# Kernel tuning notes

Hardware: AMD Instinct MI355X
Metric: run time of the kernel (lower is better)

Reference implementation:

```python
import jax, jax.numpy as jnp
import numpy as np

N, P, E = 100000, 10000, 500000
DN, DP, DK, SKIP, MLP_H = 256, 128, 100, 27, 64
E_MEAN, E_STD = 4.0, 2.0
ETA_MEAN, ETA_STD = 0.0, 1.5
ATT_NORM = 0.1  # 1/sqrt(100)
LN_EPS, RMS_EPS = 1e-5, 1e-6


def setup_inputs() -> dict:
    key = jax.random.key(0)
    ks = jax.random.split(key, 32)
    DIN = DN + SKIP  # 283
    s = 0.05
    inp = {
        'node_hidden': jax.random.normal(ks[0], (N, DN), jnp.float32),
        'energy': jax.random.uniform(ks[1], (N,), jnp.float32, 0.01, 1.0),
        'eta': jax.random.normal(ks[2], (N,), jnp.float32),
        'phi': jax.random.normal(ks[3], (N,), jnp.float32),
        'layer': jax.random.uniform(ks[4], (N,), jnp.float32),
        'eta_l': jax.random.normal(ks[5], (N, 6), jnp.float32),
        'phi_l': jax.random.normal(ks[6], (N, 6), jnp.float32),
        'ene_l': jax.random.normal(ks[7], (N, 6), jnp.float32),
        'track_feats': jax.random.uniform(ks[8], (N, 5), jnp.float32),
        'particle_hidden': jax.random.normal(ks[9], (P, DP), jnp.float32),
        'global_rep': jax.random.normal(ks[10], (P, DN), jnp.float32),
        'edge_src': jax.random.randint(ks[11], (E,), 0, N, jnp.int32),
        'edge_dst': jax.random.randint(ks[12], (E,), 0, P, jnp.int32),
        # learned params
        'W_key': jax.random.normal(ks[13], (DIN, DK), jnp.float32) * s,
        'b_key': jnp.zeros((DK,), jnp.float32),
        'W_val': jax.random.normal(ks[14], (DIN, DP), jnp.float32) * s,
        'b_val': jnp.zeros((DP,), jnp.float32),
        'W_q': jax.random.normal(ks[15], (DP + DN, DK), jnp.float32) * s,
        'b_q': jnp.zeros((DK,), jnp.float32),
        'W_ih': jax.random.normal(ks[16], (DP, 3 * DP), jnp.float32) * s,
        'b_ih': jnp.zeros((3 * DP,), jnp.float32),
        'W_hh': jax.random.normal(ks[17], (DP, 3 * DP), jnp.float32) * s,
        'b_hh': jnp.zeros((3 * DP,), jnp.float32),
        'ln_g': jnp.ones((DP,), jnp.float32),
        'ln_b': jnp.zeros((DP,), jnp.float32),
        'W1': jax.random.normal(ks[18], (DP, MLP_H), jnp.float32) * s,
        'b1': jnp.zeros((MLP_H,), jnp.float32),
        'W2': jax.random.normal(ks[19], (MLP_H, DP), jnp.float32) * s,
        'b2': jnp.zeros((DP,), jnp.float32),
        'rms_w': jnp.ones((DP,), jnp.float32),
        'lin_w': jax.random.normal(ks[20], (1, DP), jnp.float32),
    }
    return inp


def _forward(node_hidden, energy, eta, phi, layer, eta_l, phi_l, ene_l, track_feats,
             particle_hidden, global_rep,
             W_key, b_key, W_val, b_val, W_q, b_q, W_ih, b_ih, W_hh, b_hh,
             ln_g, ln_b, W1, b1, W2, b2, rms_w, lin_w, edge_src, edge_dst):
    # --- build node inputs: hidden rep + 27 skip scalars (same order as torch cat) ---
    skip = jnp.concatenate([
        ((jnp.log(energy) - E_MEAN) / E_STD)[:, None],
        ((eta - ETA_MEAN) / ETA_STD)[:, None],
        phi[:, None], layer[:, None],
        (eta_l - ETA_MEAN) / ETA_STD,  # eta_l1..l6
        phi_l, ene_l,
        track_feats,  # isTrack, nTracks, tracks_pt, nTracks_4, tracks_pt_4
    ], axis=1)  # [N, 27]
    x = jnp.concatenate([node_hidden, skip], axis=1)  # [N, 283]
    keys = x @ W_key + b_key      # [N, 100]
    vals = x @ W_val + b_val      # [N, DP]
    q = jnp.concatenate([particle_hidden, global_rep], axis=1) @ W_q + b_q  # [P, 100]

    # --- per-edge attention (note: node_update consumes RAW relu attention) ---
    att = jax.nn.relu(jnp.sum(keys[edge_src] * q[edge_dst], axis=1) * ATT_NORM)  # [E]
    msg = att[:, None] * vals[edge_src]                                          # [E, DP]
    ws = jax.ops.segment_sum(msg, edge_dst, num_segments=P)                      # [P, DP]

    # --- node update: rmsnorm * sigmoid(eltwise) gating, GRU, LN, MLP residual ---
    rms = ws * jax.lax.rsqrt(jnp.mean(ws * ws, axis=-1, keepdims=True) + RMS_EPS) * rms_w
    gated = rms * jax.nn.sigmoid(ws * lin_w)

    h = particle_hidden
    gi = gated @ W_ih + b_ih
    gh = h @ W_hh + b_hh
    i_r, i_z, i_n = jnp.split(gi, 3, axis=1)
    h_r, h_z, h_n = jnp.split(gh, 3, axis=1)
    r = jax.nn.sigmoid(i_r + h_r)
    z = jax.nn.sigmoid(i_z + h_z)
    n = jnp.tanh(i_n + r * h_n)
    h_new = (1.0 - z) * n + z * h

    mu = jnp.mean(h_new, axis=-1, keepdims=True)
    var = jnp.mean((h_new - mu) ** 2, axis=-1, keepdims=True)
    ln = (h_new - mu) * jax.lax.rsqrt(var + LN_EPS) * ln_g + ln_b
    mlp = jax.nn.relu(ln @ W1 + b1) @ W2 + b2
    return h + mlp  # updated particle 'node hidden rep'


def reference(node_hidden, energy, eta, phi, layer, eta_l, phi_l, ene_l, track_feats,
              particle_hidden, global_rep, edge_src, edge_dst,
              W_key, b_key, W_val, b_val, W_q, b_q, W_ih, b_ih, W_hh, b_hh,
              ln_g, ln_b, W1, b1, W2, b2, rms_w, lin_w):
    return _forward(node_hidden, energy, eta, phi, layer, eta_l, phi_l, ene_l, track_feats,
                    particle_hidden, global_rep,
                    W_key, b_key, W_val, b_val, W_q, b_q, W_ih, b_ih, W_hh, b_hh,
                    ln_g, ln_b, W1, b1, W2, b2, rms_w, lin_w, edge_src, edge_dst)
```

## Files before the change

kernel.cpp:

```cpp
#include <hip/hip_runtime.h>
#include <hip/hip_bf16.h>
#include <math.h>

#define THREADS 256

typedef __bf16 bf16_t;
typedef __bf16 bf16x8 __attribute__((ext_vector_type(8)));
typedef __bf16 bf16x4 __attribute__((ext_vector_type(4)));
typedef float f32x4 __attribute__((ext_vector_type(4)));

__device__ __forceinline__ float sigmoidf_(float x) { return 1.f / (1.f + expf(-x)); }

__device__ __forceinline__ void gload_lds16(const void* g, void* l) {
    __builtin_amdgcn_global_load_lds((const __attribute__((address_space(1))) void*)g,
                                     (__attribute__((address_space(3))) void*)l, 16, 0, 0);
}

__device__ __forceinline__ bf16x8 cvt8(float4 a, float4 b) {
    bf16x8 v;
    v[0] = (bf16_t)a.x; v[1] = (bf16_t)a.y; v[2] = (bf16_t)a.z; v[3] = (bf16_t)a.w;
    v[4] = (bf16_t)b.x; v[5] = (bf16_t)b.y; v[6] = (bf16_t)b.z; v[7] = (bf16_t)b.w;
    return v;
}

__global__ void prep_kernel(const float* __restrict__ W_key, const float* __restrict__ W_val,
                            const float* __restrict__ W_q, const float* __restrict__ b_key,
                            const float* __restrict__ b_val, const float* __restrict__ b_q,
                            bf16_t* __restrict__ WbfT, bf16_t* __restrict__ WqT,
                            float* __restrict__ bpn, float* __restrict__ bpq)
{
    int i = blockIdx.x * THREADS + threadIdx.x;
    const int NW = 256 * 288, NQ = 128 * 384;
    if (i < NW) {
        int c = i / 288, k = i - c * 288;
        float v = 0.f;
        if (k < 283) {
            if (c < 100) v = W_key[k * 100 + c];
            else if (c >= 128 && c < 256) v = W_val[k * 128 + (c - 128)];
        }
        WbfT[i] = (bf16_t)v;
    } else if (i < NW + NQ) {
        int j = i - NW;
        int c = j / 384, k = j - c * 384;
        WqT[j] = (bf16_t)((c < 100) ? W_q[k * 100 + c] : 0.f);
    } else if (i < NW + NQ + 256) {
        int c = i - NW - NQ;
        bpn[c] = (c < 100) ? b_key[c] : ((c >= 128 && c < 256) ? b_val[c - 128] : 0.f);
    } else if (i < NW + NQ + 256 + 128) {
        int c = i - NW - NQ - 256;
        bpq[c] = (c < 100) ? b_q[c] : 0.f;
    }
}

__global__ void prep2_kernel(const float* __restrict__ W_ih, const float* __restrict__ W_hh,
                             const float* __restrict__ b_ih, const float* __restrict__ b_hh,
                             const float* __restrict__ W1, const float* __restrict__ b1,
                             const float* __restrict__ W2,
                             bf16_t* __restrict__ BTg, bf16_t* __restrict__ W1Tp,
                             bf16_t* __restrict__ W2Tp, float* __restrict__ bgru,
                             float* __restrict__ b1p,
                             int* __restrict__ cnt, int twoP,
                             bf16_t* __restrict__ AG, int padStart, int padElems)
{
    int i = blockIdx.x * THREADS + threadIdx.x;
    const int NG = 768 * 256, N1 = 128 * 128, N2 = 128 * 128;
    const int NB = NG + N1 + N2 + 768 + 128;
    if (i < NG) {
        int c = i >> 8, k = i & 255;
        float v = 0.f;
        if (c < 384) { if (k < 128) v = W_ih[k * 384 + c]; }
        else         { if (k >= 128) v = W_hh[(k - 128) * 384 + (c - 384)]; }
        BTg[i] = (bf16_t)v;
    } else if (i < NG + N1) {
        int j = i - NG; int c = j >> 7, k = j & 127;
        W1Tp[j] = (bf16_t)((c < 64) ? W1[k * 64 + c] : 0.f);
    } else if (i < NG + N1 + N2) {
        int j = i - NG - N1; int c = j >> 7, k = j & 127;
        W2Tp[j] = (bf16_t)((k < 64) ? W2[k * 128 + c] : 0.f);
    } else if (i < NG + N1 + N2 + 768) {
        int c = i - NG - N1 - N2;
        bgru[c] = (c < 384) ? b_ih[c] : b_hh[c - 384];
    } else if (i < NB) {
        int c = i - NG - N1 - N2 - 768;
        b1p[c] = (c < 64) ? b1[c] : 0.f;
    } else if (i < NB + twoP) {
        cnt[i - NB] = 0;
    } else if (i < NB + twoP + padElems) {
        int j = i - NB - twoP;
        AG[(size_t)padStart * 256 + j] = (bf16_t)0.f;
    }
}

__global__ void skip_kernel(const float* __restrict__ energy, const float* __restrict__ eta,
                            const float* __restrict__ phi, const float* __restrict__ layer,
                            const float* __restrict__ eta_l, const float* __restrict__ phi_l,
                            const float* __restrict__ ene_l, const float* __restrict__ track,
                            bf16_t* __restrict__ skipb, int N_, int Mpad)
{
    int n = blockIdx.x * THREADS + threadIdx.x;
    if (n >= Mpad) return;
    float o[32];
#pragma unroll
    for (int j = 0; j < 32; ++j) o[j] = 0.f;
    if (n < N_) {
        o[0] = (logf(energy[n]) - 4.0f) * 0.5f;
        o[1] = eta[n] * (1.f / 1.5f);
        o[2] = phi[n];
        o[3] = layer[n];
#pragma unroll
        for (int j = 0; j < 6; ++j) o[4 + j]  = eta_l[n * 6 + j] * (1.f / 1.5f);
#pragma unroll
        for (int j = 0; j < 6; ++j) o[10 + j] = phi_l[n * 6 + j];
#pragma unroll
        for (int j = 0; j < 6; ++j) o[16 + j] = ene_l[n * 6 + j];
#pragma unroll
        for (int j = 0; j < 5; ++j) o[22 + j] = track[n * 5 + j];
    }
    bf16_t* dst = skipb + (size_t)n * 32;
#pragma unroll
    for (int g = 0; g < 4; ++g) {
        bf16x8 v;
#pragma unroll
        for (int j = 0; j < 8; ++j) v[j] = (bf16_t)o[g * 8 + j];
        *(bf16x8*)(dst + g * 8) = v;
    }
}

__global__ __launch_bounds__(256) void kv_gemm(
    const float* __restrict__ nh, const bf16_t* __restrict__ skipb,
    const bf16_t* __restrict__ BT, const float* __restrict__ bias,
    bf16_t* __restrict__ KVb, int N_)
{
    __shared__ short As[64 * 288];
    int tid = threadIdx.x;
    int w = tid >> 6, lane = tid & 63;
    int la = lane & 15, hi = lane >> 4;
    int row0 = blockIdx.x * 64;
    int col0 = w * 64;

#pragma unroll
    for (int r = 0; r < 16; ++r) {
        int row = r * 4 + w;
        int grow = row0 + row;
        float4 f = make_float4(0.f, 0.f, 0.f, 0.f);
        if (grow < N_) f = *(const float4*)(nh + (size_t)grow * 256 + lane * 4);
        bf16x4 h;
        h[0] = (bf16_t)f.x; h[1] = (bf16_t)f.y; h[2] = (bf16_t)f.z; h[3] = (bf16_t)f.w;
        *(bf16x4*)(As + row * 288 + lane * 4) = h;
    }
    {
        int row = tid >> 2, part = tid & 3;
        bf16x8 s = *(const bf16x8*)(skipb + (size_t)(row0 + row) * 32 + part * 8);
        *(bf16x8*)(As + row * 288 + 256 + part * 8) = s;
    }
    __syncthreads();

    f32x4 zero4 = {0.f, 0.f, 0.f, 0.f};
    f32x4 acc[4][4];
#pragma unroll
    for (int i = 0; i < 4; ++i)
#pragma unroll
        for (int j = 0; j < 4; ++j) acc[i][j] = zero4;

#pragma unroll
    for (int t = 0; t < 9; ++t) {
        int kt = t * 32;
        bf16x8 b[4];
#pragma unroll
        for (int j = 0; j < 4; ++j)
            b[j] = *(const bf16x8*)(BT + (size_t)(col0 + j * 16 + la) * 288 + kt + hi * 8);
        bf16x8 a[4];
#pragma unroll
        for (int i = 0; i < 4; ++i)
            a[i] = *(const bf16x8*)(As + (i * 16 + la) * 288 + kt + hi * 8);
#pragma unroll
        for (int i = 0; i < 4; ++i)
#pragma unroll
            for (int j = 0; j < 4; ++j)
                acc[i][j] = __builtin_amdgcn_mfma_f32_16x16x32_bf16(a[i], b[j], acc[i][j], 0, 0, 0);
    }

#pragma unroll
    for (int j = 0; j < 4; ++j) {
        int col = col0 + j * 16 + la;
        float bb = bias[col];
#pragma unroll
        for (int i = 0; i < 4; ++i) {
#pragma unroll
            for (int r = 0; r < 4; ++r) {
                int row = row0 + i * 16 + hi * 4 + r;
                KVb[(size_t)row * 256 + col] = (bf16_t)(acc[i][j][r] + bb);
            }
        }
    }
}

template <int MODE>
__global__ __launch_bounds__(256) void mfma_gemm(
    const void* __restrict__ A0, const void* __restrict__ A1,
    const bf16_t* __restrict__ BT, const float* __restrict__ bias,
    void* __restrict__ out0v, const float* __restrict__ resid,
    int K, int Mlimit, int Nrows)
{
    __shared__ short AsS[64 * 32];
    __shared__ short BsS[128 * 32];
    int tid = threadIdx.x;
    int lane = tid & 63, w = tid >> 6;
    int la = lane & 15, hi = lane >> 4;
    int m0 = (w & 1) * 32, n0 = (w >> 1) * 64;
    int row0 = blockIdx.y * 64, col0 = blockIdx.x * 128;

    f32x4 zero4 = {0.f, 0.f, 0.f, 0.f};
    f32x4 acc[2][4];
#pragma unroll
    for (int i = 0; i < 2; ++i)
#pragma unroll
        for (int j = 0; j < 4; ++j) acc[i][j] = zero4;

    const int ra = tid >> 2, ka = (tid & 3) * 8;
    const int c1 = tid + 256;
    const int rb0 = tid >> 2, kb0 = (tid & 3) * 8;
    const int rb1 = c1 >> 2,  kb1 = (c1 & 3) * 8;

    for (int kt = 0; kt < K; kt += 32) {
        int gmA = row0 + ra;
        if (MODE == 1) {
            int gk = kt + ka;
            bf16x8 v = {};
            if (gmA < Nrows) {
                const float* s = (gk < 128) ? ((const float*)A0 + (size_t)gmA * 128 + gk)
                                            : ((const float*)A1 + (size_t)gmA * 256 + (gk - 128));
                v = cvt8(*(const float4*)s, *(const float4*)(s + 4));
            }
            *(bf16x8*)(AsS + (size_t)tid * 8) = v;
        } else {
            gload_lds16((const bf16_t*)A0 + (size_t)gmA * K + kt + ka,
                        AsS + (size_t)tid * 8);
        }
        gload_lds16(BT + (size_t)(col0 + rb0) * K + kt + kb0, BsS + (size_t)tid * 8);
        gload_lds16(BT + (size_t)(col0 + rb1) * K + kt + kb1, BsS + (size_t)c1 * 8);
        __syncthreads();
        bf16x8 a[2], b[4];
#pragma unroll
        for (int i = 0; i < 2; ++i)
            a[i] = *(const bf16x8*)(AsS + (m0 + i * 16 + la) * 32 + hi * 8);
#pragma unroll
        for (int j = 0; j < 4; ++j)
            b[j] = *(const bf16x8*)(BsS + (n0 + j * 16 + la) * 32 + hi * 8);
#pragma unroll
        for (int i = 0; i < 2; ++i)
#pragma unroll
            for (int j = 0; j < 4; ++j)
                acc[i][j] = __builtin_amdgcn_mfma_f32_16x16x32_bf16(a[i], b[j], acc[i][j], 0, 0, 0);
        __syncthreads();
    }

#pragma unroll
    for (int i = 0; i < 2; ++i) {
#pragma unroll
        for (int j = 0; j < 4; ++j) {
            int col = col0 + n0 + j * 16 + la;
            float bb = bias[col];
#pragma unroll
            for (int r = 0; r < 4; ++r) {
                int row = row0 + m0 + i * 16 + hi * 4 + r;
                float v = acc[i][j][r] + bb;
                if (MODE == 1) {
                    ((bf16_t*)out0v)[(size_t)row * 128 + col] = (bf16_t)v;
                } else if (MODE == 2) {
                    ((float*)out0v)[(size_t)row * 768 + col] = v;
                } else if (MODE == 3) {
                    ((bf16_t*)out0v)[(size_t)row * 128 + col] = (bf16_t)fmaxf(v, 0.f);
                } else {
                    if (row < Mlimit)
                        ((float*)out0v)[(size_t)row * 128 + col] = v + resid[(size_t)row * 128 + col];
                }
            }
        }
    }
}

__global__ void hist_kernel(const int* __restrict__ dst, int* __restrict__ cnt, int E_)
{
    int i = blockIdx.x * THREADS + threadIdx.x;
    if (i < E_) atomicAdd(&cnt[dst[i]], 1);
}

__global__ void scan_kernel(const int* __restrict__ cnt, int* __restrict__ offb, int P_)
{
    __shared__ int wsum[16];
    int tid = threadIdx.x;
    int lane = tid & 63, w = tid >> 6;
    int base = tid * 10;
    int c[10];
    int s = 0;
#pragma unroll
    for (int j = 0; j < 10; ++j) {
        int i = base + j;
        c[j] = (i < P_) ? cnt[i] : 0;
        s += c[j];
    }
    int pre = s;
    for (int o = 1; o < 64; o <<= 1) {
        int t = __shfl_up(pre, o);
        if (lane >= o) pre += t;
    }
    if (lane == 63) wsum[w] = pre;
    __syncthreads();
    if (w == 0 && lane < 16) {
        int v = wsum[lane];
        for (int o = 1; o < 16; o <<= 1) {
            int t = __shfl_up(v, o, 16);
            if (lane >= o) v += t;
        }
        wsum[lane] = v;
    }
    __syncthreads();
    int waveoff = (w == 0) ? 0 : wsum[w - 1];
    int run = waveoff + pre - s;
#pragma unroll
    for (int j = 0; j < 10; ++j) {
        int i = base + j;
        if (i <= P_) offb[i] = run;
        run += c[j];
    }
}

__global__ void fill_src_kernel(const int* __restrict__ dst, const int* __restrict__ src,
                                const int* __restrict__ offb, int* __restrict__ cur,
                                int* __restrict__ csrc, int E_)
{
    int i = blockIdx.x * THREADS + threadIdx.x;
    if (i < E_) {
        int d = dst[i];
        int pos = atomicAdd(&cur[d], 1);
        csrc[offb[d] + pos] = src[i];
    }
}

__global__ __launch_bounds__(256) void edge_kernel(
    const int* __restrict__ offb, const int* __restrict__ csrc,
    const bf16_t* __restrict__ KVb, const bf16_t* __restrict__ Qb,
    const float* __restrict__ ph, const float* __restrict__ rms_w,
    const float* __restrict__ lin_w, bf16_t* __restrict__ AG, int P_)
{
    int tid = threadIdx.x;
    int p = blockIdx.x * 4 + (tid >> 6);
    if (p >= P_) return;
    int lane = tid & 63;
    int c = lane & 15, g = lane >> 4;

    bf16x8 q8 = *(const bf16x8*)(Qb + (size_t)p * 128 + c * 8);
    float qf[8];
#pragma unroll
    for (int j = 0; j < 8; ++j) qf[j] = (float)q8[j];

    int s0 = offb[p], e0 = offb[p + 1];
    float acc[8] = {};

    int i = s0 + g;
    for (; i + 12 < e0; i += 16) {
        int n0 = csrc[i], n1 = csrc[i + 4], n2 = csrc[i + 8], n3 = csrc[i + 12];
        const bf16_t* b0 = KVb + (size_t)n0 * 256 + c * 8;
        const bf16_t* b1 = KVb + (size_t)n1 * 256 + c * 8;
        const bf16_t* b2 = KVb + (size_t)n2 * 256 + c * 8;
        const bf16_t* b3 = KVb + (size_t)n3 * 256 + c * 8;
        bf16x8 k0 = *(const bf16x8*)b0, v0 = *(const bf16x8*)(b0 + 128);
        bf16x8 k1 = *(const bf16x8*)b1, v1 = *(const bf16x8*)(b1 + 128);
        bf16x8 k2 = *(const bf16x8*)b2, v2 = *(const bf16x8*)(b2 + 128);
        bf16x8 k3 = *(const bf16x8*)b3, v3 = *(const bf16x8*)(b3 + 128);
        float d0 = 0.f, d1 = 0.f, d2 = 0.f, d3 = 0.f;
#pragma unroll
        for (int j = 0; j < 8; ++j) {
            d0 += qf[j] * (float)k0[j]; d1 += qf[j] * (float)k1[j];
            d2 += qf[j] * (float)k2[j]; d3 += qf[j] * (float)k3[j];
        }
        d0 += __shfl_xor(d0, 1); d1 += __shfl_xor(d1, 1); d2 += __shfl_xor(d2, 1); d3 += __shfl_xor(d3, 1);
        d0 += __shfl_xor(d0, 2); d1 += __shfl_xor(d1, 2); d2 += __shfl_xor(d2, 2); d3 += __shfl_xor(d3, 2);
        d0 += __shfl_xor(d0, 4); d1 += __shfl_xor(d1, 4); d2 += __shfl_xor(d2, 4); d3 += __shfl_xor(d3, 4);
        d0 += __shfl_xor(d0, 8); d1 += __shfl_xor(d1, 8); d2 += __shfl_xor(d2, 8); d3 += __shfl_xor(d3, 8);
        float a0 = fmaxf(d0 * 0.1f, 0.f), a1 = fmaxf(d1 * 0.1f, 0.f);
        float a2 = fmaxf(d2 * 0.1f, 0.f), a3 = fmaxf(d3 * 0.1f, 0.f);
#pragma unroll
        for (int j = 0; j < 8; ++j)
            acc[j] += a0 * (float)v0[j] + a1 * (float)v1[j]
                    + a2 * (float)v2[j] + a3 * (float)v3[j];
    }
    for (; i < e0; i += 4) {
        int nA = csrc[i];
        const bf16_t* bA = KVb + (size_t)nA * 256 + c * 8;
        bf16x8 kA = *(const bf16x8*)bA;
        bf16x8 vA = *(const bf16x8*)(bA + 128);
        float dA = 0.f;
#pragma unroll
        for (int j = 0; j < 8; ++j) dA += qf[j] * (float)kA[j];
        dA += __shfl_xor(dA, 1);
        dA += __shfl_xor(dA, 2);
        dA += __shfl_xor(dA, 4);
        dA += __shfl_xor(dA, 8);
        float aA = fmaxf(dA * 0.1f, 0.f);
#pragma unroll
        for (int j = 0; j < 8; ++j) acc[j] += aA * (float)vA[j];
    }

#pragma unroll
    for (int j = 0; j < 8; ++j) {
        acc[j] += __shfl_xor(acc[j], 16);
        acc[j] += __shfl_xor(acc[j], 32);
    }

    float ss = 0.f;
#pragma unroll
    for (int j = 0; j < 8; ++j) ss += acc[j] * acc[j];
    ss += __shfl_xor(ss, 1); ss += __shfl_xor(ss, 2); ss += __shfl_xor(ss, 4); ss += __shfl_xor(ss, 8);
    float scale = rsqrtf(ss * (1.f / 128.f) + 1e-6f);
    if (g == 0) {
        int cb = c * 8;
        const float* hp = ph + (size_t)p * 128 + cb;
        float4 ha = *(const float4*)hp, hb = *(const float4*)(hp + 4);
        float hv[8] = {ha.x, ha.y, ha.z, ha.w, hb.x, hb.y, hb.z, hb.w};
        bf16x8 gv, hvb;
#pragma unroll
        for (int j = 0; j < 8; ++j) {
            float wsv = acc[j];
            float rv = wsv * scale * rms_w[cb + j];
            gv[j] = (bf16_t)(rv * sigmoidf_(wsv * lin_w[cb + j]));
            hvb[j] = (bf16_t)hv[j];
        }
        *(bf16x8*)(AG + (size_t)p * 256 + cb) = gv;
        *(bf16x8*)(AG + (size_t)p * 256 + 128 + cb) = hvb;
    }
}

__global__ void gru_ln_kernel(const float* __restrict__ G768, const float* __restrict__ ph,
                              const float* __restrict__ ln_g, const float* __restrict__ ln_b,
                              bf16_t* __restrict__ LNb, int P_, int Mq)
{
    int tid = threadIdx.x;
    int g = tid >> 4, s = tid & 15;
    int p = blockIdx.x * 16 + g;
    if (p >= Mq) return;
    int cb = s * 8;
    if (p >= P_) {
        bf16x8 z = {};
        *(bf16x8*)(LNb + (size_t)p * 128 + cb) = z;
        return;
    }
    const float* G = G768 + (size_t)p * 768;
    float ir[8], iz[8], in_[8], hr[8], hz[8], hn_[8], hv[8];
#pragma unroll
    for (int q = 0; q < 2; ++q) {
        float4 v;
        v = *(const float4*)(G + cb + q * 4);        ir[q*4]=v.x; ir[q*4+1]=v.y; ir[q*4+2]=v.z; ir[q*4+3]=v.w;
        v = *(const float4*)(G + 128 + cb + q * 4);  iz[q*4]=v.x; iz[q*4+1]=v.y; iz[q*4+2]=v.z; iz[q*4+3]=v.w;
        v = *(const float4*)(G + 256 + cb + q * 4);  in_[q*4]=v.x; in_[q*4+1]=v.y; in_[q*4+2]=v.z; in_[q*4+3]=v.w;
        v = *(const float4*)(G + 384 + cb + q * 4);  hr[q*4]=v.x; hr[q*4+1]=v.y; hr[q*4+2]=v.z; hr[q*4+3]=v.w;
        v = *(const float4*)(G + 512 + cb + q * 4);  hz[q*4]=v.x; hz[q*4+1]=v.y; hz[q*4+2]=v.z; hz[q*4+3]=v.w;
        v = *(const float4*)(G + 640 + cb + q * 4);  hn_[q*4]=v.x; hn_[q*4+1]=v.y; hn_[q*4+2]=v.z; hn_[q*4+3]=v.w;
        v = *(const float4*)(ph + (size_t)p * 128 + cb + q * 4);
        hv[q*4]=v.x; hv[q*4+1]=v.y; hv[q*4+2]=v.z; hv[q*4+3]=v.w;
    }
    float hn[8];
    float sm = 0.f, sq = 0.f;
#pragma unroll
    for (int j = 0; j < 8; ++j) {
        float r = sigmoidf_(ir[j] + hr[j]);
        float z = sigmoidf_(iz[j] + hz[j]);
        float n = tanhf(in_[j] + r * hn_[j]);
        hn[j] = (1.f - z) * n + z * hv[j];
        sm += hn[j]; sq += hn[j] * hn[j];
    }
    sm += __shfl_xor(sm, 1); sm += __shfl_xor(sm, 2); sm += __shfl_xor(sm, 4); sm += __shfl_xor(sm, 8);
    sq += __shfl_xor(sq, 1); sq += __shfl_xor(sq, 2); sq += __shfl_xor(sq, 4); sq += __shfl_xor(sq, 8);
    float mu = sm * (1.f / 128.f);
    float var = sq * (1.f / 128.f) - mu * mu;
    float iv = rsqrtf(var + 1e-5f);
    bf16x8 o;
#pragma unroll
    for (int j = 0; j < 8; ++j) {
        int c = cb + j;
        o[j] = (bf16_t)((hn[j] - mu) * iv * ln_g[c] + ln_b[c]);
    }
    *(bf16x8*)(LNb + (size_t)p * 128 + cb) = o;
}

extern "C" void kernel_launch(void* const* d_in, const int* in_sizes, int n_in,
                              void* d_out, int out_size, void* d_ws, size_t ws_size,
                              hipStream_t stream)
{
    const float* nh      = (const float*)d_in[0];
    const float* energy  = (const float*)d_in[1];
    const float* eta     = (const float*)d_in[2];
    const float* phi     = (const float*)d_in[3];
    const float* layer   = (const float*)d_in[4];
    const float* eta_l   = (const float*)d_in[5];
    const float* phi_l   = (const float*)d_in[6];
    const float* ene_l   = (const float*)d_in[7];
    const float* track   = (const float*)d_in[8];
    const float* ph      = (const float*)d_in[9];
    const float* grep    = (const float*)d_in[10];
    const int*   esrc    = (const int*)d_in[11];
    const int*   edst    = (const int*)d_in[12];
    const float* W_key   = (const float*)d_in[13];
    const float* b_key   = (const float*)d_in[14];
    const float* W_val   = (const float*)d_in[15];
    const float* b_val   = (const float*)d_in[16];
    const float* W_q     = (const float*)d_in[17];
    const float* b_q     = (const float*)d_in[18];
    const float* W_ih    = (const float*)d_in[19];
    const float* b_ih    = (const float*)d_in[20];
    const float* W_hh    = (const float*)d_in[21];
    const float* b_hh    = (const float*)d_in[22];
    const float* ln_g    = (const float*)d_in[23];
    const float* ln_b    = (const float*)d_in[24];
    const float* W1      = (const float*)d_in[25];
    const float* b1      = (const float*)d_in[26];
    const float* W2      = (const float*)d_in[27];
    const float* b2      = (const float*)d_in[28];
    const float* rms_w   = (const float*)d_in[29];
    const float* lin_w   = (const float*)d_in[30];

    const int N = in_sizes[1];
    const int P = in_sizes[9] / 128;
    const int E = in_sizes[11];
    const int Mpad = ((N + 127) / 128) * 128;
    const int Mq   = ((P + 127) / 128) * 128;

    char* base = (char*)d_ws;
    size_t off = 0;
    auto alloc = [&](size_t bytes) { void* p = base + off; off = (off + bytes + 255) & ~(size_t)255; return p; };
    bf16_t* skipb = (bf16_t*)alloc((size_t)Mpad * 32 * 2);
    bf16_t* WbfT  = (bf16_t*)alloc(256 * 288 * 2);
    bf16_t* WqT   = (bf16_t*)alloc(128 * 384 * 2);
    float*  bpn   = (float*)alloc(256 * 4);
    float*  bpq   = (float*)alloc(128 * 4);
    bf16_t* KVb   = (bf16_t*)alloc((size_t)Mpad * 256 * 2);
    bf16_t* Qb    = (bf16_t*)alloc((size_t)Mq * 128 * 2);
    int*    cnt   = (int*)alloc((size_t)(2 * P) * 4);
    int*    cur   = cnt + P;
    int*    offb  = (int*)alloc((size_t)(P + 1) * 4);
    int*    csrc  = (int*)alloc((size_t)E * 4);
    bf16_t* AG    = (bf16_t*)alloc((size_t)Mq * 256 * 2);
    bf16_t* BTg   = (bf16_t*)alloc(768 * 256 * 2);
    bf16_t* W1Tp  = (bf16_t*)alloc(128 * 128 * 2);
    bf16_t* W2Tp  = (bf16_t*)alloc(128 * 128 * 2);
    float*  bgru  = (float*)alloc(768 * 4);
    float*  b1p   = (float*)alloc(128 * 4);
    float*  G768  = (float*)alloc((size_t)Mq * 768 * 4);
    bf16_t* LNb   = (bf16_t*)alloc((size_t)Mq * 128 * 2);
    bf16_t* M1    = (bf16_t*)alloc((size_t)Mq * 128 * 2);

    {
        int total = 256 * 288 + 128 * 384 + 256 + 128;
        prep_kernel<<<(total + THREADS - 1) / THREADS, THREADS, 0, stream>>>(
            W_key, W_val, W_q, b_key, b_val, b_q, WbfT, WqT, bpn, bpq);
        int padElems = (Mq - P) * 256;
        int total2 = 768 * 256 + 128 * 128 + 128 * 128 + 768 + 128 + 2 * P + padElems;
        prep2_kernel<<<(total2 + THREADS - 1) / THREADS, THREADS, 0, stream>>>(
            W_ih, W_hh, b_ih, b_hh, W1, b1, W2, BTg, W1Tp, W2Tp, bgru, b1p,
            cnt, 2 * P, AG, P, padElems);
        skip_kernel<<<(Mpad + THREADS - 1) / THREADS, THREADS, 0, stream>>>(
            energy, eta, phi, layer, eta_l, phi_l, ene_l, track, skipb, N, Mpad);
    }
    kv_gemm<<<Mpad / 64, THREADS, 0, stream>>>(nh, skipb, WbfT, bpn, KVb, N);
    mfma_gemm<1><<<dim3(1, Mq / 64), THREADS, 0, stream>>>(
        ph, grep, WqT, bpq, Qb, nullptr, 384, 0, P);
    hist_kernel<<<(E + THREADS - 1) / THREADS, THREADS, 0, stream>>>(edst, cnt, E);
    scan_kernel<<<1, 1024, 0, stream>>>(cnt, offb, P);
    fill_src_kernel<<<(E + THREADS - 1) / THREADS, THREADS, 0, stream>>>(
        edst, esrc, offb, cur, csrc, E);
    edge_kernel<<<(P + 3) / 4, THREADS, 0, stream>>>(
        offb, csrc, KVb, Qb, ph, rms_w, lin_w, AG, P);
    mfma_gemm<2><<<dim3(6, Mq / 64), THREADS, 0, stream>>>(
        AG, nullptr, BTg, bgru, G768, nullptr, 256, 0, Mq);
    gru_ln_kernel<<<Mq / 16, THREADS, 0, stream>>>(G768, ph, ln_g, ln_b, LNb, P, Mq);
    mfma_gemm<3><<<dim3(1, Mq / 64), THREADS, 0, stream>>>(
        LNb, nullptr, W1Tp, b1p, M1, nullptr, 128, 0, Mq);
    mfma_gemm<4><<<dim3(1, Mq / 64), THREADS, 0, stream>>>(
        M1, nullptr, W2Tp, b2, d_out, ph, 128, P, Mq);
}
```

Baseline: 226.1 us.

## Pre-pack KV weight fragments and pad LDS row stride in kv_gemm

Adds a prep kernel that rearranges the transposed KV weight into MFMA-fragment order, so each lane's B-operand load in kv_gemm becomes a contiguous coalesced 16-byte read instead of a strided one across rows. It also pads the shared-memory A tile row stride from 288 to 296 elements to reduce LDS bank conflicts on the A fragment reads. The cost is one extra small prep launch and a little more LDS per block.

Measured after the change: 224.4 us. Within noise of the previous version (-0.8%).

```diff
diff --git a/kernel.cpp b/kernel.cpp
--- a/kernel.cpp
+++ b/kernel.cpp
@@ -50,6 +50,21 @@
         int c = i - NW - NQ - 256;
         bpq[c] = (c < 100) ? b_q[c] : 0.f;
     }
+}
+
+__global__ void prep3_kernel(const bf16_t* __restrict__ WbfT, bf16_t* __restrict__ Bpack)
+{
+    int i = blockIdx.x * THREADS + threadIdx.x;
+    const int TOT = 4 * 9 * 4 * 512;
+    if (i >= TOT) return;
+    int frag = i >> 9, e = i & 511;
+    int l = e >> 3, c8 = e & 7;
+    int w = frag / 36, rem = frag - w * 36;
+    int t = rem >> 2, j = rem & 3;
+    int la = l & 15, hi = l >> 4;
+    int col = w * 64 + j * 16 + la;
+    int k = t * 32 + hi * 8 + c8;
+    Bpack[i] = WbfT[col * 288 + k];
 }
 
 __global__ void prep2_kernel(const float* __restrict__ W_ih, const float* __restrict__ W_hh,
@@ -128,10 +143,11 @@
 
 __global__ __launch_bounds__(256) void kv_gemm(
     const float* __restrict__ nh, const bf16_t* __restrict__ skipb,
-    const bf16_t* __restrict__ BT, const float* __restrict__ bias,
+    const bf16_t* __restrict__ Bpack, const float* __restrict__ bias,
     bf16_t* __restrict__ KVb, int N_)
 {
-    __shared__ short As[64 * 288];
+    const int LD = 296;
+    __shared__ short As[64 * 296];
     int tid = threadIdx.x;
     int w = tid >> 6, lane = tid & 63;
     int la = lane & 15, hi = lane >> 4;
@@ -146,12 +162,12 @@
         if (grow < N_) f = *(const float4*)(nh + (size_t)grow * 256 + lane * 4);
         bf16x4 h;
         h[0] = (bf16_t)f.x; h[1] = (bf16_t)f.y; h[2] = (bf16_t)f.z; h[3] = (bf16_t)f.w;
-        *(bf16x4*)(As + row * 288 + lane * 4) = h;
+        *(bf16x4*)(As + row * LD + lane * 4) = h;
     }
     {
         int row = tid >> 2, part = tid & 3;
         bf16x8 s = *(const bf16x8*)(skipb + (size_t)(row0 + row) * 32 + part * 8);
-        *(bf16x8*)(As + row * 288 + 256 + part * 8) = s;
+        *(bf16x8*)(As + row * LD + 256 + part * 8) = s;
     }
     __syncthreads();
 
@@ -162,17 +178,18 @@
 #pragma unroll
         for (int j = 0; j < 4; ++j) acc[i][j] = zero4;
 
+    const bf16_t* bp = Bpack + (size_t)(w * 9) * 4 * 512 + lane * 8;
 #pragma unroll
     for (int t = 0; t < 9; ++t) {
         int kt = t * 32;
         bf16x8 b[4];
 #pragma unroll
         for (int j = 0; j < 4; ++j)
-            b[j] = *(const bf16x8*)(BT + (size_t)(col0 + j * 16 + la) * 288 + kt + hi * 8);
+            b[j] = *(const bf16x8*)(bp + (size_t)(t * 4 + j) * 512);
         bf16x8 a[4];
 #pragma unroll
         for (int i = 0; i < 4; ++i)
-            a[i] = *(const bf16x8*)(As + (i * 16 + la) * 288 + kt + hi * 8);
+            a[i] = *(const bf16x8*)(As + (i * 16 + la) * LD + kt + hi * 8);
 #pragma unroll
         for (int i = 0; i < 4; ++i)
 #pragma unroll
@@ -531,6 +548,7 @@
     auto alloc = [&](size_t bytes) { void* p = base + off; off = (off + bytes + 255) & ~(size_t)255; return p; };
     bf16_t* skipb = (bf16_t*)alloc((size_t)Mpad * 32 * 2);
     bf16_t* WbfT  = (bf16_t*)alloc(256 * 288 * 2);
+    bf16_t* Bpack = (bf16_t*)alloc(4 * 9 * 4 * 512 * 2);
     bf16_t* WqT   = (bf16_t*)alloc(128 * 384 * 2);
     float*  bpn   = (float*)alloc(256 * 4);
     float*  bpq   = (float*)alloc(128 * 4);
@@ -554,6 +572,8 @@
         int total = 256 * 288 + 128 * 384 + 256 + 128;
         prep_kernel<<<(total + THREADS - 1) / THREADS, THREADS, 0, stream>>>(
             W_key, W_val, W_q, b_key, b_val, b_q, WbfT, WqT, bpn, bpq);
+        prep3_kernel<<<(4 * 9 * 4 * 512 + THREADS - 1) / THREADS, THREADS, 0, stream>>>(
+            WbfT, Bpack);
         int padElems = (Mq - P) * 256;
         int total2 = 768 * 256 + 128 * 128 + 128 * 128 + 768 + 128 + 2 * P + padElems;
         prep2_kernel<<<(total2 + THREADS - 1) / THREADS, THREADS, 0, stream>>>(
@@ -562,7 +582,7 @@
         skip_kernel<<<(Mpad + THREADS - 1) / THREADS, THREADS, 0, stream>>>(
             energy, eta, phi, layer, eta_l, phi_l, ene_l, track, skipb, N, Mpad);
     }
-    kv_gemm<<<Mpad / 64, THREADS, 0, stream>>>(nh, skipb, WbfT, bpn, KVb, N);
+    kv_gemm<<<Mpad / 64, THREADS, 0, stream>>>(nh, skipb, Bpack, bpn, KVb, N);
     mfma_gemm<1><<<dim3(1, Mq / 64), THREADS, 0, stream>>>(
         ph, grep, WqT, bpq, Qb, nullptr, 384, 0, P);
     hist_kernel<<<(E + THREADS - 1) / THREADS, THREADS, 0, stream>>>(edst, cnt, E);
```
